# Kernel optimization log

Measured on AMD Instinct MI355X. Metric: run time of the kernel, lower is better.

## Reference

```python
import jax, jax.numpy as jnp
from jax import lax
import numpy as np

B, T, H = 8192, 1024, 10


def setup_inputs() -> dict:
    key = jax.random.key(0)
    ks = jax.random.split(key, 7)
    s = 1.0 / np.sqrt(H)  # PyTorch default init scale for LSTM/Linear
    return {
        "x": jax.random.normal(ks[0], (B, T, 1), dtype=jnp.float32),
        "W_ih": jax.random.uniform(ks[1], (4 * H, 1), jnp.float32, -s, s),
        "W_hh": jax.random.uniform(ks[2], (4 * H, H), jnp.float32, -s, s),
        "b_ih": jax.random.uniform(ks[3], (4 * H,), jnp.float32, -s, s),
        "b_hh": jax.random.uniform(ks[4], (4 * H,), jnp.float32, -s, s),
        "W_lin": jax.random.uniform(ks[5], (1, H), jnp.float32, -s, s),
        "b_lin": jax.random.uniform(ks[6], (1,), jnp.float32, -s, s),
    }


def reference(x, W_ih, W_hh, b_ih, b_hh, W_lin, b_lin):
    # x: [B, T, 1] (batch_first). PyTorch gate order: i, f, g, o.
    b = b_ih + b_hh  # [4H]
    # Precompute input projections for all timesteps: [T, B, 4H]
    xg = jnp.einsum("bti,gi->tbg", x, W_ih) + b

    def step(carry, xg_t):
        h, c = carry  # each [B, H]
        gates = xg_t + h @ W_hh.T  # [B, 4H]
        i, f, g, o = jnp.split(gates, 4, axis=-1)
        c = jax.nn.sigmoid(f) * c + jax.nn.sigmoid(i) * jnp.tanh(g)
        h = jax.nn.sigmoid(o) * jnpp_tanh(c) if False else jax.nn.sigmoid(o) * jnp.tanh(c)
        return (h, c), None

    h0 = jnp.zeros((x.shape[0], W_hh.shape[1]), x.dtype)
    (_, cT), _ = lax.scan(step, (h0, h0), xg)
    # Module uses the final CELL state c_n, reshaped to [B, H], then Linear(10,1)
    return cT @ W_lin.T + b_lin  # [B, 1]
```

## Files before the change

kernel.cpp:

```cpp
#include <hip/hip_runtime.h>

#define B_TOT 8192
#define T_LEN 1024
#define HID 10
#define BPW 6

typedef float v2f __attribute__((ext_vector_type(2)));

__global__ __launch_bounds__(64) void lstm_fused_kernel(
    const float* __restrict__ x,
    const float* __restrict__ W_ih,
    const float* __restrict__ W_hh,
    const float* __restrict__ b_ih,
    const float* __restrict__ b_hh,
    const float* __restrict__ W_lin,
    const float* __restrict__ b_lin,
    float* __restrict__ out)
{
    const int lane = threadIdx.x;
    const int grp  = lane / HID;
    const int j    = lane - grp * HID;
    const int grpc = grp < BPW ? grp : BPW - 1;
    const int b    = blockIdx.x * BPW + grpc;
    const int bc   = b < B_TOT ? b : B_TOT - 1;
    const bool act = (grp < BPW) && (b < B_TOT);

    const int pbase = 4 * HID * grpc;

    const float NL = -1.4426950408889634f;
    const float TL =  2.8853900817779268f;

    v2f w01[HID], w23[HID];
    v2f wi01, wi23, b01, b23;
    {
        const int r0 = 0 * HID + j, r1 = 1 * HID + j;
        const int r2 = 2 * HID + j, r3 = 3 * HID + j;
        wi01 = (v2f){NL * W_ih[r0], NL * W_ih[r1]};
        wi23 = (v2f){TL * W_ih[r2], NL * W_ih[r3]};
        b01  = (v2f){NL * (b_ih[r0] + b_hh[r0]), NL * (b_ih[r1] + b_hh[r1])};
        b23  = (v2f){TL * (b_ih[r2] + b_hh[r2]), NL * (b_ih[r3] + b_hh[r3])};
#pragma unroll
        for (int k = 0; k < HID; ++k) {
            w01[k] = (v2f){NL * W_hh[r0 * HID + k], NL * W_hh[r1 * HID + k]};
            w23[k] = (v2f){TL * W_hh[r2 * HID + k], NL * W_hh[r3 * HID + k]};
        }
    }
    const float wl = W_lin[j] * 0.34657359027997264f;

    float h = 0.0f, C = 0.0f;
    const float* xb = x + (size_t)bc * T_LEN;

#define BC(K) __int_as_float(__builtin_amdgcn_ds_bpermute(pbase + 4 * (K), hbits))

#define ACC(K, HK, A01, A23)                                                  \
    {                                                                         \
        v2f hk2 = (v2f){(HK), (HK)};                                          \
        A01 = __builtin_elementwise_fma(w01[K], hk2, A01);                    \
        A23 = __builtin_elementwise_fma(w23[K], hk2, A23);                    \
    }

#define LSTM_STEP(xv)                                                         \
    {                                                                         \
        const int hbits = __float_as_int(h);                                  \
        float hk0 = BC(0), hk1 = BC(1), hk2_ = BC(2), hk3 = BC(3);            \
        float hk4 = BC(4), hk5 = BC(5), hk6 = BC(6), hk7 = BC(7);             \
        float hk8 = BC(8), hk9 = BC(9);                                       \
        v2f xv2 = (v2f){(xv), (xv)};                                          \
        v2f a01 = __builtin_elementwise_fma(xv2, wi01, b01);                  \
        v2f a23 = __builtin_elementwise_fma(xv2, wi23, b23);                  \
        v2f s01 = (v2f){0.0f, 0.0f}, s23 = (v2f){0.0f, 0.0f};                 \
        ACC(0, hk0, a01, a23) ACC(1, hk1, a01, a23) ACC(2, hk2_, a01, a23)    \
        ACC(3, hk3, a01, a23) ACC(4, hk4, a01, a23)                           \
        ACC(5, hk5, s01, s23) ACC(6, hk6, s01, s23) ACC(7, hk7, s01, s23)     \
        ACC(8, hk8, s01, s23) ACC(9, hk9, s01, s23)                           \
        a01 += s01;                                                           \
        a23 += s23;                                                           \
        float ig = __builtin_amdgcn_rcpf(1.0f + __builtin_amdgcn_exp2f(a01.x)); \
        float fg = __builtin_amdgcn_rcpf(1.0f + __builtin_amdgcn_exp2f(a01.y)); \
        float rg = __builtin_amdgcn_rcpf(1.0f + __builtin_amdgcn_exp2f(a23.x)); \
        float og = __builtin_amdgcn_rcpf(1.0f + __builtin_amdgcn_exp2f(a23.y)); \
        float gg = fmaf(-2.0f * TL, rg, TL);              \
        C = fmaf(fg, C, ig * gg);                                             \
        float tc = fmaf(-2.0f,                                                \
                        __builtin_amdgcn_rcpf(1.0f + __builtin_amdgcn_exp2f(C)), \
                        1.0f);                                                \
        h = og * tc;                                                          \
    }

    float4 xq = *reinterpret_cast<const float4*>(xb);
    int t = 0;
    for (; t < T_LEN - 4; t += 4) {
        float4 xn = *reinterpret_cast<const float4*>(xb + t + 4);
        LSTM_STEP(xq.x)
        LSTM_STEP(xq.y)
        LSTM_STEP(xq.z)
        LSTM_STEP(xq.w)
        xq = xn;
    }
    LSTM_STEP(xq.x)
    LSTM_STEP(xq.y)
    LSTM_STEP(xq.z)
    LSTM_STEP(xq.w)

#undef LSTM_STEP
#undef ACC
#undef BC

    __shared__ float red[64];
    red[lane] = act ? C * wl : 0.0f;
    __syncthreads();
    if (act && j == 0) {
        float s = b_lin[0];
#pragma unroll
        for (int u = 0; u < HID; ++u) s += red[grpc * HID + u];
        out[b] = s;
    }
}

extern "C" void kernel_launch(void* const* d_in, const int* in_sizes, int n_in,
                              void* d_out, int out_size, void* d_ws, size_t ws_size,
                              hipStream_t stream) {
    const float* x     = (const float*)d_in[0];
    const float* W_ih  = (const float*)d_in[1];
    const float* W_hh  = (const float*)d_in[2];
    const float* b_ih  = (const float*)d_in[3];
    const float* b_hh  = (const float*)d_in[4];
    const float* W_lin = (const float*)d_in[5];
    const float* b_lin = (const float*)d_in[6];
    float* out = (float*)d_out;

    dim3 grid((B_TOT + BPW - 1) / BPW), block(64);
    hipLaunchKernelGGL(lstm_fused_kernel, grid, block, 0, stream,
                       x, W_ih, W_hh, b_ih, b_hh, W_lin, b_lin, out);
}
```

Baseline: 333.4 us.

## Broadcast hidden state via LDS and merge sigmoid-tanh reciprocals

Each lane now writes its hidden value to shared memory and reads its group's ten h values as five float2 loads, replacing ten ds_bpermute broadcasts per step. The gate math is rewritten so sigmoid(i)*tanh(g) and sigmoid(o)*tanh(c) each use a single reciprocal of a product. That cuts the per-step transcendental count on the serial recurrence path. fminf clamps at 80 keep the exponentials from overflowing. The packed v2f FMAs become scalar FMAs, doubling the FMA instruction count. The LDS exchange and the final reduction now rely on single-wavefront lockstep with no barrier.

Measured after the change: 355.6 us. 1.07x slower.

```diff
diff --git a/kernel.cpp b/kernel.cpp
--- a/kernel.cpp
+++ b/kernel.cpp
@@ -4,8 +4,6 @@
 #define T_LEN 1024
 #define HID 10
 #define BPW 6
-
-typedef float v2f __attribute__((ext_vector_type(2)));
 
 __global__ __launch_bounds__(64) void lstm_fused_kernel(
     const float* __restrict__ x,
@@ -20,71 +18,80 @@
     const int lane = threadIdx.x;
     const int grp  = lane / HID;
     const int j    = lane - grp * HID;
-    const int grpc = grp < BPW ? grp : BPW - 1;
-    const int b    = blockIdx.x * BPW + grpc;
-    const int bc   = b < B_TOT ? b : B_TOT - 1;
-    const bool act = (grp < BPW) && (b < B_TOT);
+    const bool act = (lane < BPW * HID);
+    const int g    = act ? grp : (BPW - 1);
+    const int jj   = act ? j : 0;
+    const int b    = blockIdx.x * BPW + g;
+    const bool bok = act && (b < B_TOT);
+    const int bc   = (b < B_TOT) ? b : (B_TOT - 1);
+    const int rbase = g * HID;
 
-    const int pbase = 4 * HID * grpc;
+    __shared__ float sh[64];
 
     const float NL = -1.4426950408889634f;
     const float TL =  2.8853900817779268f;
 
-    v2f w01[HID], w23[HID];
-    v2f wi01, wi23, b01, b23;
+    float w0[HID], w1[HID], w2[HID], w3[HID];
+    float wi0, wi1, wi2, wi3, bb0, bb1, bb2, bb3;
     {
-        const int r0 = 0 * HID + j, r1 = 1 * HID + j;
-        const int r2 = 2 * HID + j, r3 = 3 * HID + j;
-        wi01 = (v2f){NL * W_ih[r0], NL * W_ih[r1]};
-        wi23 = (v2f){TL * W_ih[r2], NL * W_ih[r3]};
-        b01  = (v2f){NL * (b_ih[r0] + b_hh[r0]), NL * (b_ih[r1] + b_hh[r1])};
-        b23  = (v2f){TL * (b_ih[r2] + b_hh[r2]), NL * (b_ih[r3] + b_hh[r3])};
+        const int r0 = 0*HID+jj, r1 = 1*HID+jj, r2 = 2*HID+jj, r3 = 3*HID+jj;
+        wi0 = NL*W_ih[r0]; wi1 = NL*W_ih[r1]; wi2 = TL*W_ih[r2]; wi3 = NL*W_ih[r3];
+        bb0 = NL*(b_ih[r0]+b_hh[r0]); bb1 = NL*(b_ih[r1]+b_hh[r1]);
+        bb2 = TL*(b_ih[r2]+b_hh[r2]); bb3 = NL*(b_ih[r3]+b_hh[r3]);
 #pragma unroll
         for (int k = 0; k < HID; ++k) {
-            w01[k] = (v2f){NL * W_hh[r0 * HID + k], NL * W_hh[r1 * HID + k]};
-            w23[k] = (v2f){TL * W_hh[r2 * HID + k], NL * W_hh[r3 * HID + k]};
+            w0[k] = NL*W_hh[r0*HID+k];
+            w1[k] = NL*W_hh[r1*HID+k];
+            w2[k] = TL*W_hh[r2*HID+k];
+            w3[k] = NL*W_hh[r3*HID+k];
         }
     }
-    const float wl = W_lin[j] * 0.34657359027997264f;
+    const float wl = W_lin[jj] * 0.34657359027997264f;
 
     float h = 0.0f, C = 0.0f;
     const float* xb = x + (size_t)bc * T_LEN;
 
-#define BC(K) __int_as_float(__builtin_amdgcn_ds_bpermute(pbase + 4 * (K), hbits))
-
-#define ACC(K, HK, A01, A23)                                                  \
-    {                                                                         \
-        v2f hk2 = (v2f){(HK), (HK)};                                          \
-        A01 = __builtin_elementwise_fma(w01[K], hk2, A01);                    \
-        A23 = __builtin_elementwise_fma(w23[K], hk2, A23);                    \
-    }
-
 #define LSTM_STEP(xv)                                                         \
     {                                                                         \
-        const int hbits = __float_as_int(h);                                  \
-        float hk0 = BC(0), hk1 = BC(1), hk2_ = BC(2), hk3 = BC(3);            \
-        float hk4 = BC(4), hk5 = BC(5), hk6 = BC(6), hk7 = BC(7);             \
-        float hk8 = BC(8), hk9 = BC(9);                                       \
-        v2f xv2 = (v2f){(xv), (xv)};                                          \
-        v2f a01 = __builtin_elementwise_fma(xv2, wi01, b01);                  \
-        v2f a23 = __builtin_elementwise_fma(xv2, wi23, b23);                  \
-        v2f s01 = (v2f){0.0f, 0.0f}, s23 = (v2f){0.0f, 0.0f};                 \
-        ACC(0, hk0, a01, a23) ACC(1, hk1, a01, a23) ACC(2, hk2_, a01, a23)    \
-        ACC(3, hk3, a01, a23) ACC(4, hk4, a01, a23)                           \
-        ACC(5, hk5, s01, s23) ACC(6, hk6, s01, s23) ACC(7, hk7, s01, s23)     \
-        ACC(8, hk8, s01, s23) ACC(9, hk9, s01, s23)                           \
-        a01 += s01;                                                           \
-        a23 += s23;                                                           \
-        float ig = __builtin_amdgcn_rcpf(1.0f + __builtin_amdgcn_exp2f(a01.x)); \
-        float fg = __builtin_amdgcn_rcpf(1.0f + __builtin_amdgcn_exp2f(a01.y)); \
-        float rg = __builtin_amdgcn_rcpf(1.0f + __builtin_amdgcn_exp2f(a23.x)); \
-        float og = __builtin_amdgcn_rcpf(1.0f + __builtin_amdgcn_exp2f(a23.y)); \
-        float gg = fmaf(-2.0f * TL, rg, TL);              \
-        C = fmaf(fg, C, ig * gg);                                             \
-        float tc = fmaf(-2.0f,                                                \
-                        __builtin_amdgcn_rcpf(1.0f + __builtin_amdgcn_exp2f(C)), \
-                        1.0f);                                                \
-        h = og * tc;                                                          \
+        sh[lane] = h;             \
+        const float2* hp = (const float2*)(sh + rbase);                       \
+        float2 p0 = hp[0], p1 = hp[1], p2 = hp[2], p3 = hp[3], p4 = hp[4];    \
+        float a0 = fmaf((xv), wi0, bb0);                                      \
+        float a1 = fmaf((xv), wi1, bb1);                                      \
+        float a2 = fmaf((xv), wi2, bb2);                                      \
+        float a3 = fmaf((xv), wi3, bb3);                                      \
+        a0 = fmaf(w0[0],p0.x,a0); a1 = fmaf(w1[0],p0.x,a1);                   \
+        a2 = fmaf(w2[0],p0.x,a2); a3 = fmaf(w3[0],p0.x,a3);                   \
+        a0 = fmaf(w0[1],p0.y,a0); a1 = fmaf(w1[1],p0.y,a1);                   \
+        a2 = fmaf(w2[1],p0.y,a2); a3 = fmaf(w3[1],p0.y,a3);                   \
+        a0 = fmaf(w0[2],p1.x,a0); a1 = fmaf(w1[2],p1.x,a1);                   \
+        a2 = fmaf(w2[2],p1.x,a2); a3 = fmaf(w3[2],p1.x,a3);                   \
+        a0 = fmaf(w0[3],p1.y,a0); a1 = fmaf(w1[3],p1.y,a1);                   \
+        a2 = fmaf(w2[3],p1.y,a2); a3 = fmaf(w3[3],p1.y,a3);                   \
+        a0 = fmaf(w0[4],p2.x,a0); a1 = fmaf(w1[4],p2.x,a1);                   \
+        a2 = fmaf(w2[4],p2.x,a2); a3 = fmaf(w3[4],p2.x,a3);                   \
+        a0 = fmaf(w0[5],p2.y,a0); a1 = fmaf(w1[5],p2.y,a1);                   \
+        a2 = fmaf(w2[5],p2.y,a2); a3 = fmaf(w3[5],p2.y,a3);                   \
+        float s0 = w0[6]*p3.x, s1 = w1[6]*p3.x, s2 = w2[6]*p3.x, s3 = w3[6]*p3.x; \
+        s0 = fmaf(w0[7],p3.y,s0); s1 = fmaf(w1[7],p3.y,s1);                   \
+        s2 = fmaf(w2[7],p3.y,s2); s3 = fmaf(w3[7],p3.y,s3);                   \
+        s0 = fmaf(w0[8],p4.x,s0); s1 = fmaf(w1[8],p4.x,s1);                   \
+        s2 = fmaf(w2[8],p4.x,s2); s3 = fmaf(w3[8],p4.x,s3);                   \
+        s0 = fmaf(w0[9],p4.y,s0); s1 = fmaf(w1[9],p4.y,s1);                   \
+        s2 = fmaf(w2[9],p4.y,s2); s3 = fmaf(w3[9],p4.y,s3);                   \
+        a0 += s0; a1 += s1; a3 += s3;                                         \
+        a2 = fminf(a2 + s2, 80.0f);                                           \
+        float ei = __builtin_amdgcn_exp2f(a0);                                \
+        float ef = __builtin_amdgcn_exp2f(a1);                                \
+        float eg = __builtin_amdgcn_exp2f(a2);                                \
+        float eo = __builtin_amdgcn_exp2f(a3);                                \
+        float fg = __builtin_amdgcn_rcpf(1.0f + ef);                          \
+        float rp = __builtin_amdgcn_rcpf((1.0f + ei) * (1.0f + eg));          \
+        float igg = (eg - 1.0f) * rp * TL;           \
+        C = fminf(fmaf(fg, C, igg), 80.0f);                                   \
+        float eC = __builtin_amdgcn_exp2f(C);                                 \
+        float rq = __builtin_amdgcn_rcpf((1.0f + eo) * (1.0f + eC));          \
+        h = (eC - 1.0f) * rq;                             \
     }
 
     float4 xq = *reinterpret_cast<const float4*>(xb);
@@ -101,18 +108,13 @@
     LSTM_STEP(xq.y)
     LSTM_STEP(xq.z)
     LSTM_STEP(xq.w)
+#undef LSTM_STEP
 
-#undef LSTM_STEP
-#undef ACC
-#undef BC
-
-    __shared__ float red[64];
-    red[lane] = act ? C * wl : 0.0f;
-    __syncthreads();
-    if (act && j == 0) {
+    sh[lane] = bok ? C * wl : 0.0f;
+    if (bok && j == 0) {
         float s = b_lin[0];
 #pragma unroll
-        for (int u = 0; u < HID; ++u) s += red[grpc * HID + u];
+        for (int u = 0; u < HID; ++u) s += sh[rbase + u];
         out[b] = s;
     }
 }
```
